# Kernel optimization log

Measured on AMD Instinct MI355X. Metric: run time of the kernel, lower is better.

## Reference

```python
import jax, jax.numpy as jnp
import numpy as np

B, N, C, H = 4, 2048, 768, 12
D = C // H  # head_dim = 64


def setup_inputs() -> dict:
    key = jax.random.key(0)
    ks = jax.random.split(key, 16)
    s = 1.0 / np.sqrt(C)
    inp = {
        "x1": jax.random.normal(ks[0], (B, N, C), jnp.float32),
        "x2": jax.random.normal(ks[1], (B, N, C), jnp.float32),
        "mask_1": jax.random.uniform(ks[2], (B, N), jnp.float32),
        "mask_2": jax.random.uniform(ks[3], (B, N), jnp.float32),
        "Wq": jax.random.normal(ks[4], (C, C), jnp.float32) * s,
        "bq": jnp.zeros((C,), jnp.float32),
        "Wk": jax.random.normal(ks[5], (C, C), jnp.float32) * s,
        "bk": jnp.zeros((C,), jnp.float32),
        "Wv": jax.random.normal(ks[6], (C, C), jnp.float32) * s,
        "bv": jnp.zeros((C,), jnp.float32),
        "Wo": jax.random.normal(ks[7], (C, C), jnp.float32) * s,
        "bo": jnp.zeros((C,), jnp.float32),
        "temperature": jnp.asarray(1.0, jnp.float32),
        "ln_gamma": jnp.ones((C,), jnp.float32),
        "ln_beta": jnp.zeros((C,), jnp.float32),
    }
    return inp


def _layernorm(x, gamma, beta, eps=1e-5):
    mu = jnp.mean(x, axis=-1, keepdims=True)
    var = jnp.var(x, axis=-1, keepdims=True)
    return (x - mu) * jax.lax.rsqrt(var + eps) * gamma + beta


def reference(x1, x2, mask_1, mask_2, Wq, bq, Wk, bk, Wv, bv, Wo, bo,
              temperature, ln_gamma, ln_beta):
    # projections (nn.Linear: x @ W^T + b)
    q = (x1 @ Wq.T + bq).reshape(B, N, H, D).transpose(0, 2, 1, 3)  # [B,H,N,D]
    k = (x2 @ Wk.T + bk).reshape(B, N, H, D).transpose(0, 2, 1, 3)
    v = (x2 @ Wv.T + bv).reshape(B, N, H, D).transpose(0, 2, 1, 3)

    scores = jnp.einsum("bhnd,bhmd->bhnm", q, k) / jnp.sqrt(jnp.float32(D))
    # relative confidence bias: (mask_1[b,n] - mask_2[b,m]) / temperature
    rel = (mask_1[:, :, None] - mask_2[:, None, :]) / temperature  # [B,N,N]
    scores = scores + rel[:, None, :, :]

    attn = jax.nn.softmax(scores, axis=-1)  # dropout = identity (eval mode)
    out = jnp.einsum("bhnm,bhmd->bhnd", attn, v)
    out = out.transpose(0, 2, 1, 3).reshape(B, N, C)
    out = out @ Wo.T + bo
    return _layernorm(0.5 * x1 + out, ln_gamma, ln_beta)
```

## Files before the change

### kernel.cpp

```cpp
#include <hip/hip_runtime.h>
#include <stdint.h>

#define B_ 4
#define N_ 2048
#define C_ 768
#define H_ 12
#define D_ 64
#define NTOK 8192

typedef short bf16x8 __attribute__((ext_vector_type(8)));
typedef float f32x4 __attribute__((ext_vector_type(4)));
typedef float f32x16 __attribute__((ext_vector_type(16)));
typedef unsigned short ushort8 __attribute__((ext_vector_type(8)));
typedef unsigned short u16x4 __attribute__((ext_vector_type(4)));

__device__ __forceinline__ unsigned short f2bf(float f) {
  union { float f; unsigned u; } v; v.f = f;
  unsigned r = v.u + 0x7FFFu + ((v.u >> 16) & 1u);
  return (unsigned short)(r >> 16);
}

__device__ __forceinline__ void load_lds16(const void* g, void* lds_base) {
  __builtin_amdgcn_global_load_lds(
      (const __attribute__((address_space(1))) unsigned int*)g,
      (__attribute__((address_space(3))) unsigned int*)(uint32_t)(uintptr_t)lds_base,
      16, 0, 0);
}

__device__ __forceinline__ int fswz(int r) { return (r + (r >> 3)) & 7; }

__device__ __forceinline__ bf16x8 pack8t(const float* p) {
  union { unsigned u[4]; bf16x8 v; } r;
#pragma unroll
  for (int j=0;j<4;j++) {
    union { float f; unsigned u; } a, b;
    a.f = p[2*j]; b.f = p[2*j+1];
    r.u[j] = __builtin_amdgcn_perm(b.u, a.u, 0x07060302u);
  }
  return r.v;
}

__global__ __launch_bounds__(256) void cvt6(
    const float* s0, const float* s1, const float* s2, const float* s3,
    const float* s4, const float* s5,
    unsigned short* d0, unsigned short* d1, unsigned short* d2,
    unsigned short* d3, unsigned short* d4, unsigned short* d5,
    const float* mask2, const float* temp, float* u,
    int n01, int n25)
{
  int y = blockIdx.y;
  int i = (blockIdx.x*256 + threadIdx.x)*8;
  if (y == 6) {
    if (i >= NTOK) return;
    const float nsc = -1.4426950408889634f / temp[0];
    float4 f0 = *(const float4*)(mask2+i);
    float4 f1 = *(const float4*)(mask2+i+4);
    float4 o0, o1;
    o0.x = __builtin_amdgcn_exp2f(f0.x*nsc); o0.y = __builtin_amdgcn_exp2f(f0.y*nsc);
    o0.z = __builtin_amdgcn_exp2f(f0.z*nsc); o0.w = __builtin_amdgcn_exp2f(f0.w*nsc);
    o1.x = __builtin_amdgcn_exp2f(f1.x*nsc); o1.y = __builtin_amdgcn_exp2f(f1.y*nsc);
    o1.z = __builtin_amdgcn_exp2f(f1.z*nsc); o1.w = __builtin_amdgcn_exp2f(f1.w*nsc);
    *(float4*)(u+i) = o0;
    *(float4*)(u+i+4) = o1;
    return;
  }
  const float* s = (y==0)?s0:(y==1)?s1:(y==2)?s2:(y==3)?s3:(y==4)?s4:s5;
  unsigned short* d = (y==0)?d0:(y==1)?d1:(y==2)?d2:(y==3)?d3:(y==4)?d4:d5;
  int n = (y<2) ? n01 : n25;
  if (i >= n) return;
  float4 f0 = *(const float4*)(s+i);
  float4 f1 = *(const float4*)(s+i+4);
  ushort8 o;
  o[0]=f2bf(f0.x); o[1]=f2bf(f0.y); o[2]=f2bf(f0.z); o[3]=f2bf(f0.w);
  o[4]=f2bf(f1.x); o[5]=f2bf(f1.y); o[6]=f2bf(f1.z); o[7]=f2bf(f1.w);
  *(ushort8*)(d+i) = o;
}

__device__ __forceinline__ void gemm_core(const unsigned short* A, const unsigned short* W,
                                          int rowBase, int colBase, f32x4 (&acc)[4][4],
                                          unsigned short* As, unsigned short* Bs)
{
  int tid = threadIdx.x, wave = tid>>6, lane = tid&63, quad = lane>>4, l16 = lane&15;
  int wm = wave>>1, wn = wave&1;
  for (int k0 = 0; k0 < 768; k0 += 32) {
    __syncthreads();
#pragma unroll
    for (int p = 0; p < 2; ++p) {
      int c = p*256 + wave*64 + lane;
      load_lds16(A + (size_t)(rowBase + (c>>2))*768 + k0 + (c&3)*8,
                 As + (size_t)(p*256 + wave*64)*8);
      load_lds16(W + (size_t)(colBase + (c>>2))*768 + k0 + (c&3)*8,
                 Bs + (size_t)(p*256 + wave*64)*8);
    }
    __syncthreads();
    bf16x8 af[4], bw[4];
#pragma unroll
    for (int i=0;i<4;i++) af[i] = *(const bf16x8*)(As + (wm*64 + i*16 + l16)*32 + quad*8);
#pragma unroll
    for (int j=0;j<4;j++) bw[j] = *(const bf16x8*)(Bs + (wn*64 + j*16 + l16)*32 + quad*8);
#pragma unroll
    for (int i=0;i<4;i++)
#pragma unroll
      for (int j=0;j<4;j++)
        acc[i][j] = __builtin_amdgcn_mfma_f32_16x16x32_bf16(af[i], bw[j], acc[i][j], 0,0,0);
  }
}

__global__ __launch_bounds__(256) void qkv_gemm(
    const unsigned short* xb1, const unsigned short* xb2,
    const unsigned short* Wq, const unsigned short* Wk, const unsigned short* Wv,
    const float* bq, const float* bk, const float* bv, const float* u,
    unsigned short* Qb, unsigned short* Kb, unsigned short* Vt)
{
  __shared__ unsigned short As[128*32];
  __shared__ unsigned short Bs[128*32];
  int z = blockIdx.z;
  const unsigned short* A = (z==0) ? xb1 : xb2;
  const unsigned short* W = (z==0) ? Wq : (z==1) ? Wk : Wv;
  const float* bias       = (z==0) ? bq : (z==1) ? bk : bv;
  int rowBase = blockIdx.x*128, colBase = blockIdx.y*128;
  int tid = threadIdx.x, wave = tid>>6, lane = tid&63, quad = lane>>4, l16 = lane&15;
  int wm = wave>>1, wn = wave&1;
  f32x4 acc[4][4] = {};
  gemm_core(A, W, rowBase, colBase, acc, As, Bs);
  if (z == 2) {
#pragma unroll
    for (int i=0;i<4;i++) {
      int m0 = rowBase + wm*64 + i*16 + quad*4;
      float4 uv = *(const float4*)(u + m0);
      int b = m0 >> 11, n0 = m0 & 2047;
      int slotbase = (n0 & ~63) | (i*16) | ((quad&1)<<3) | ((quad>>1)<<2);
#pragma unroll
      for (int j=0;j<4;j++) {
        int col = colBase + wn*64 + j*16 + l16;
        float bv_ = bias[col];
        int h = col >> 6, d = col & 63;
        u16x4 o;
        o[0] = f2bf((acc[i][j][0] + bv_) * uv.x);
        o[1] = f2bf((acc[i][j][1] + bv_) * uv.y);
        o[2] = f2bf((acc[i][j][2] + bv_) * uv.z);
        o[3] = f2bf((acc[i][j][3] + bv_) * uv.w);
        *(u16x4*)(Vt + (((size_t)b*H_ + h)*D_ + d)*(size_t)N_ + slotbase) = o;
      }
    }
  } else {
    unsigned short* out = (z==0) ? Qb : Kb;
    float qs = (z==0) ? 0.18033688011112042f : 1.0f;
#pragma unroll
    for (int i=0;i<4;i++)
#pragma unroll
      for (int j=0;j<4;j++) {
        int col = colBase + wn*64 + j*16 + l16;
        float bv_ = bias[col];
        int h = col >> 6, d = col & 63;
#pragma unroll
        for (int r=0;r<4;r++) {
          int m = rowBase + wm*64 + i*16 + quad*4 + r;
          int b = m >> 11, n = m & 2047;
          out[(((size_t)b*H_ + h)*N_ + n)*D_ + d] = f2bf((acc[i][j][r] + bv_) * qs);
        }
      }
  }
}

__device__ __forceinline__ void attn_stage(const unsigned short* Kb, const unsigned short* Vtg,
                                           size_t bh, int kt, int tid, int wave,
                                           unsigned short* KsBuf, unsigned short* VsBuf)
{
#pragma unroll
  for (int p=0;p<2;p++) {
    int idx = p*256 + tid;
    int key = idx >> 3, c = idx & 7;
    load_lds16(Kb + (bh*N_ + (size_t)kt*64 + key)*D_ + (c ^ fswz(key))*8,
               KsBuf + (size_t)(p*256 + wave*64)*8);
  }
#pragma unroll
  for (int p=0;p<2;p++) {
    int idx = p*256 + tid;
    int d = idx >> 3, c = idx & 7;
    load_lds16(Vtg + (bh*D_ + d)*(size_t)N_ + kt*64 + (c ^ fswz(d))*8,
               VsBuf + (size_t)(p*256 + wave*64)*8);
  }
}

__global__ __launch_bounds__(256) void attn_kernel(
    const unsigned short* Qb, const unsigned short* Kb, const unsigned short* Vtg,
    const float* u, unsigned short* Ob)
{
  __shared__ unsigned short Ks[2][64*64];
  __shared__ unsigned short Vs[2][64*64];
  __shared__ float us[N_];
  int bx = blockIdx.x;
  int xcd = bx & 7, slot = bx >> 3;
  int bh_i = xcd*6 + (slot >> 4);
  int qt = slot & 15;
  int b = bh_i / H_, h = bh_i - b*H_;
  int tid = threadIdx.x, wave = tid>>6, lane = tid&63;
  int l32 = lane & 31, hl = lane >> 5;
  size_t bh = (size_t)bh_i;
  int qrow = qt*128 + wave*32 + l32;
  int fsb = l32 + (l32 >> 3);

#pragma unroll
  for (int r=0;r<2;r++) {
    int i = (r*256 + tid)*4;
    *(float4*)(us+i) = *(const float4*)(u + (size_t)b*N_ + i);
  }

  bf16x8 qf[4];
  const unsigned short* Qp = Qb + (bh*N_ + qrow)*D_;
#pragma unroll
  for (int i=0;i<4;i++) qf[i] = *(const bf16x8*)(Qp + i*16 + hl*8);

  float lrun = 0.f;
  f32x16 oacc0 = {}, oacc1 = {};

  attn_stage(Kb, Vtg, bh, 0, tid, wave, Ks[0], Vs[0]);
  __syncthreads();

  for (int kt = 0; kt < N_/64; ++kt) {
    int cur = kt & 1;
    if (kt+1 < N_/64)
      attn_stage(Kb, Vtg, bh, kt+1, tid, wave, Ks[cur^1], Vs[cur^1]);
    const unsigned short* Kc = Ks[cur];
    const unsigned short* Vc = Vs[cur];
#pragma unroll
    for (int sub=0; sub<2; ++sub) {
      f32x16 sa = {};
#pragma unroll
      for (int i=0;i<4;i++) {
        int ch = (2*i + hl) ^ ((fsb + 4*sub) & 7);
        bf16x8 kf = *(const bf16x8*)(Kc + (sub*32 + l32)*64 + ch*8);
        sa = __builtin_amdgcn_mfma_f32_32x32x16_bf16(kf, qf[i], sa, 0,0,0);
      }
      float pv[16];
      float la[4];
#pragma unroll
      for (int g=0; g<4; ++g) {
        float4 uv = *(const float4*)(us + kt*64 + sub*32 + g*8 + hl*4);
        float p0 = __builtin_amdgcn_exp2f(sa[g*4+0]);
        float p1 = __builtin_amdgcn_exp2f(sa[g*4+1]);
        float p2 = __builtin_amdgcn_exp2f(sa[g*4+2]);
        float p3 = __builtin_amdgcn_exp2f(sa[g*4+3]);
        pv[g*4+0]=p0; pv[g*4+1]=p1; pv[g*4+2]=p2; pv[g*4+3]=p3;
        la[g] = fmaf(p0, uv.x, fmaf(p1, uv.y, fmaf(p2, uv.z, p3*uv.w)));
      }
      lrun += (la[0]+la[1]) + (la[2]+la[3]);
      bf16x8 pf0 = pack8t(pv);
      bf16x8 pf1 = pack8t(pv+8);
#pragma unroll
      for (int kc=0;kc<2;kc++) {
        bf16x8 pf = kc ? pf1 : pf0;
        int m = sub*2 + kc;
        int chv = (2*m + hl) ^ (fsb & 7);
        oacc0 = __builtin_amdgcn_mfma_f32_32x32x16_bf16(
                  *(const bf16x8*)(Vc + l32*64 + chv*8), pf, oacc0, 0,0,0);
        int chv1 = (2*m + hl) ^ ((fsb + 4) & 7);
        oacc1 = __builtin_amdgcn_mfma_f32_32x32x16_bf16(
                  *(const bf16x8*)(Vc + (32+l32)*64 + chv1*8), pf, oacc1, 0,0,0);
      }
    }
    __syncthreads();
  }

  lrun += __shfl_xor(lrun, 32);
  float rinv = 1.0f / lrun;
  size_t obase = ((size_t)b*N_ + qrow)*C_ + h*D_;
#pragma unroll
  for (int dh=0; dh<2; ++dh)
#pragma unroll
    for (int g=0; g<4; ++g) {
      int d = dh*32 + g*8 + hl*4;
      u16x4 o;
#pragma unroll
      for (int q=0;q<4;q++) {
        float val = (dh==0 ? oacc0[g*4+q] : oacc1[g*4+q]) * rinv;
        o[q] = f2bf(val);
      }
      *(u16x4*)(Ob + obase + d) = o;
    }
}

__global__ __launch_bounds__(256) void out_gemm(
    const unsigned short* Ob, const unsigned short* Wo, const float* bo,
    const float* x1, float* Z)
{
  __shared__ unsigned short As[128*32];
  __shared__ unsigned short Bs[128*32];
  int rowBase = blockIdx.x*128, colBase = blockIdx.y*128;
  int tid = threadIdx.x, wave = tid>>6, lane = tid&63, quad = lane>>4, l16 = lane&15;
  int wm = wave>>1, wn = wave&1;
  f32x4 acc[4][4] = {};
  gemm_core(Ob, Wo, rowBase, colBase, acc, As, Bs);
#pragma unroll
  for (int i=0;i<4;i++)
#pragma unroll
    for (int j=0;j<4;j++) {
      int col = colBase + wn*64 + j*16 + l16;
      float bv_ = bo[col];
#pragma unroll
      for (int r=0;r<4;r++) {
        size_t m = rowBase + wm*64 + i*16 + quad*4 + r;
        Z[m*768 + col] = acc[i][j][r] + bv_ + 0.5f*x1[m*768 + col];
      }
    }
}

__global__ __launch_bounds__(256) void ln_kernel(const float* Z, const float* gam,
                                                 const float* bet, float* out)
{
  size_t row = blockIdx.x;
  int t = threadIdx.x;
  const float* z = Z + row*768;
  float v0 = z[t], v1 = z[t+256], v2 = z[t+512];
  float s = v0+v1+v2;
  float ss = v0*v0 + v1*v1 + v2*v2;
#pragma unroll
  for (int off=1; off<64; off<<=1) { s += __shfl_xor(s, off); ss += __shfl_xor(ss, off); }
  __shared__ float red[8];
  int wave = t>>6, lane = t&63;
  if (lane==0) { red[wave] = s; red[4+wave] = ss; }
  __syncthreads();
  float S = red[0]+red[1]+red[2]+red[3];
  float SS = red[4]+red[5]+red[6]+red[7];
  float mean = S * (1.0f/768.0f);
  float var = SS * (1.0f/768.0f) - mean*mean;
  float rstd = rsqrtf(var + 1e-5f);
  float* o = out + row*768;
  o[t]     = (v0-mean)*rstd*gam[t]     + bet[t];
  o[t+256] = (v1-mean)*rstd*gam[t+256] + bet[t+256];
  o[t+512] = (v2-mean)*rstd*gam[t+512] + bet[t+512];
}

extern "C" void kernel_launch(void* const* d_in, const int* in_sizes, int n_in,
                              void* d_out, int out_size, void* d_ws, size_t ws_size,
                              hipStream_t stream)
{
  const float* x1    = (const float*)d_in[0];
  const float* x2    = (const float*)d_in[1];
  const float* mask2 = (const float*)d_in[3];
  const float* Wq    = (const float*)d_in[4];
  const float* bq    = (const float*)d_in[5];
  const float* Wk    = (const float*)d_in[6];
  const float* bk    = (const float*)d_in[7];
  const float* Wv    = (const float*)d_in[8];
  const float* bv    = (const float*)d_in[9];
  const float* Wo    = (const float*)d_in[10];
  const float* bo    = (const float*)d_in[11];
  const float* temp  = (const float*)d_in[12];
  const float* gam   = (const float*)d_in[13];
  const float* bet   = (const float*)d_in[14];

  char* ws = (char*)d_ws;
  size_t off = 0;
  auto alloc = [&](size_t bytes) { void* p = ws + off; off += (bytes + 255) & ~255ull; return p; };
  const size_t XB = (size_t)NTOK * C_ * 2;
  const size_t WB = (size_t)C_ * C_ * 2;
  unsigned short* xb1 = (unsigned short*)alloc(XB);
  unsigned short* xb2 = (unsigned short*)alloc(XB);
  unsigned short* Wqb = (unsigned short*)alloc(WB);
  unsigned short* Wkb = (unsigned short*)alloc(WB);
  unsigned short* Wvb = (unsigned short*)alloc(WB);
  unsigned short* Wob = (unsigned short*)alloc(WB);
  unsigned short* Qb  = (unsigned short*)alloc(XB);
  unsigned short* Kb  = (unsigned short*)alloc(XB);
  unsigned short* Vt  = (unsigned short*)alloc(XB);
  unsigned short* Ob  = (unsigned short*)alloc(XB);
  float* u = (float*)alloc((size_t)NTOK * 4);
  float* Z = (float*)xb1;

  cvt6<<<dim3(3072, 7), 256, 0, stream>>>(x1, x2, Wq, Wk, Wv, Wo,
                                          xb1, xb2, Wqb, Wkb, Wvb, Wob,
                                          mask2, temp, u,
                                          NTOK*C_, C_*C_);
  qkv_gemm<<<dim3(64, 6, 3), 256, 0, stream>>>(xb1, xb2, Wqb, Wkb, Wvb,
                                               bq, bk, bv, u, Qb, Kb, Vt);
  attn_kernel<<<dim3(768), 256, 0, stream>>>(Qb, Kb, Vt, u, Ob);
  out_gemm<<<dim3(64, 6), 256, 0, stream>>>(Ob, Wob, bo, x1, Z);
  ln_kernel<<<dim3(8192), 256, 0, stream>>>(Z, gam, bet, (float*)d_out);
}
```

Measured before the change: 291.8 us.

## Deepen GEMM K-tile to 64 with XOR-swizzled LDS and compact conversion grid

The shared GEMM core now stages 64-wide K slices instead of 32. It uses an XOR swizzle on 16-byte chunks so the wider LDS rows avoid bank conflicts, which halves the number of barrier pairs per tile. The fp32-to-bf16 conversion kernel moves from a 3072x7 grid, where most weight-row blocks exited early, to a flat grid of exactly the blocks needed. The cost is double the LDS per block, which may reduce occupancy.

```diff
diff --git a/kernel.cpp b/kernel.cpp
--- a/kernel.cpp
+++ b/kernel.cpp
@@ -45,13 +45,11 @@
     const float* s4, const float* s5,
     unsigned short* d0, unsigned short* d1, unsigned short* d2,
     unsigned short* d3, unsigned short* d4, unsigned short* d5,
-    const float* mask2, const float* temp, float* u,
-    int n01, int n25)
-{
-  int y = blockIdx.y;
-  int i = (blockIdx.x*256 + threadIdx.x)*8;
-  if (y == 6) {
-    if (i >= NTOK) return;
+    const float* mask2, const float* temp, float* u)
+{
+  int bid = blockIdx.x;
+  if (bid >= 7296) {
+    int i = ((bid - 7296)*256 + threadIdx.x)*8;
     const float nsc = -1.4426950408889634f / temp[0];
     float4 f0 = *(const float4*)(mask2+i);
     float4 f1 = *(const float4*)(mask2+i+4);
@@ -64,10 +62,16 @@
     *(float4*)(u+i+4) = o1;
     return;
   }
-  const float* s = (y==0)?s0:(y==1)?s1:(y==2)?s2:(y==3)?s3:(y==4)?s4:s5;
-  unsigned short* d = (y==0)?d0:(y==1)?d1:(y==2)?d2:(y==3)?d3:(y==4)?d4:d5;
-  int n = (y<2) ? n01 : n25;
-  if (i >= n) return;
+  const float* s; unsigned short* d; int i;
+  if (bid < 3072)      { s = s0; d = d0; i = (bid*256 + threadIdx.x)*8; }
+  else if (bid < 6144) { s = s1; d = d1; i = ((bid-3072)*256 + threadIdx.x)*8; }
+  else {
+    int t = bid - 6144;
+    int w = t / 288, lb = t - w*288;
+    s = (w==0)?s2:(w==1)?s3:(w==2)?s4:s5;
+    d = (w==0)?d2:(w==1)?d3:(w==2)?d4:d5;
+    i = (lb*256 + threadIdx.x)*8;
+  }
   float4 f0 = *(const float4*)(s+i);
   float4 f1 = *(const float4*)(s+i+4);
   ushort8 o;
@@ -82,27 +86,32 @@
 {
   int tid = threadIdx.x, wave = tid>>6, lane = tid&63, quad = lane>>4, l16 = lane&15;
   int wm = wave>>1, wn = wave&1;
-  for (int k0 = 0; k0 < 768; k0 += 32) {
+  for (int k0 = 0; k0 < 768; k0 += 64) {
     __syncthreads();
 #pragma unroll
-    for (int p = 0; p < 2; ++p) {
+    for (int p = 0; p < 4; ++p) {
       int c = p*256 + wave*64 + lane;
-      load_lds16(A + (size_t)(rowBase + (c>>2))*768 + k0 + (c&3)*8,
+      int row = c >> 3, ch = (c & 7) ^ (row & 7);
+      load_lds16(A + (size_t)(rowBase + row)*768 + k0 + ch*8,
                  As + (size_t)(p*256 + wave*64)*8);
-      load_lds16(W + (size_t)(colBase + (c>>2))*768 + k0 + (c&3)*8,
+      load_lds16(W + (size_t)(colBase + row)*768 + k0 + ch*8,
                  Bs + (size_t)(p*256 + wave*64)*8);
     }
     __syncthreads();
-    bf16x8 af[4], bw[4];
-#pragma unroll
-    for (int i=0;i<4;i++) af[i] = *(const bf16x8*)(As + (wm*64 + i*16 + l16)*32 + quad*8);
-#pragma unroll
-    for (int j=0;j<4;j++) bw[j] = *(const bf16x8*)(Bs + (wn*64 + j*16 + l16)*32 + quad*8);
-#pragma unroll
-    for (int i=0;i<4;i++)
-#pragma unroll
-      for (int j=0;j<4;j++)
-        acc[i][j] = __builtin_amdgcn_mfma_f32_16x16x32_bf16(af[i], bw[j], acc[i][j], 0,0,0);
+#pragma unroll
+    for (int kk = 0; kk < 2; ++kk) {
+      bf16x8 af[4], bw[4];
+      int cp = ((kk*4 + quad) ^ (l16 & 7)) * 8;
+#pragma unroll
+      for (int i=0;i<4;i++) af[i] = *(const bf16x8*)(As + (wm*64 + i*16 + l16)*64 + cp);
+#pragma unroll
+      for (int j=0;j<4;j++) bw[j] = *(const bf16x8*)(Bs + (wn*64 + j*16 + l16)*64 + cp);
+#pragma unroll
+      for (int i=0;i<4;i++)
+#pragma unroll
+        for (int j=0;j<4;j++)
+          acc[i][j] = __builtin_amdgcn_mfma_f32_16x16x32_bf16(af[i], bw[j], acc[i][j], 0,0,0);
+    }
   }
 }
 
@@ -112,8 +121,8 @@
     const float* bq, const float* bk, const float* bv, const float* u,
     unsigned short* Qb, unsigned short* Kb, unsigned short* Vt)
 {
-  __shared__ unsigned short As[128*32];
-  __shared__ unsigned short Bs[128*32];
+  __shared__ unsigned short As[128*64];
+  __shared__ unsigned short Bs[128*64];
   int z = blockIdx.z;
   const unsigned short* A = (z==0) ? xb1 : xb2;
   const unsigned short* W = (z==0) ? Wq : (z==1) ? Wk : Wv;
@@ -285,8 +294,8 @@
     const unsigned short* Ob, const unsigned short* Wo, const float* bo,
     const float* x1, float* Z)
 {
-  __shared__ unsigned short As[128*32];
-  __shared__ unsigned short Bs[128*32];
+  __shared__ unsigned short As[128*64];
+  __shared__ unsigned short Bs[128*64];
   int rowBase = blockIdx.x*128, colBase = blockIdx.y*128;
   int tid = threadIdx.x, wave = tid>>6, lane = tid&63, quad = lane>>4, l16 = lane&15;
   int wm = wave>>1, wn = wave&1;
@@ -369,10 +378,9 @@
   float* u = (float*)alloc((size_t)NTOK * 4);
   float* Z = (float*)xb1;
 
-  cvt6<<<dim3(3072, 7), 256, 0, stream>>>(x1, x2, Wq, Wk, Wv, Wo,
-                                          xb1, xb2, Wqb, Wkb, Wvb, Wob,
-                                          mask2, temp, u,
-                                          NTOK*C_, C_*C_);
+  cvt6<<<dim3(7300), 256, 0, stream>>>(x1, x2, Wq, Wk, Wv, Wo,
+                                       xb1, xb2, Wqb, Wkb, Wvb, Wob,
+                                       mask2, temp, u);
   qkv_gemm<<<dim3(64, 6, 3), 256, 0, stream>>>(xb1, xb2, Wqb, Wkb, Wvb,
                                                bq, bk, bv, u, Qb, Kb, Vt);
   attn_kernel<<<dim3(768), 256, 0, stream>>>(Qb, Kb, Vt, u, Ob);
```

Result: slower. 314.5 us (+7.8%).
